# Kernel tuning notes

Hardware: AMD Instinct MI355X
Metric: run time of the kernel (lower is better)

## Reference

```python
import jax, jax.numpy as jnp
import numpy as np

B = 2
D = 256
NH = 8
DH = D // NH
LV = 4
NP_ = 4
NL = 6
DFF = 1024
SHAPES = [(112, 112), (56, 56), (28, 28), (14, 14)]
S = sum(h * w for h, w in SHAPES)


def setup_inputs() -> dict:
    key = jax.random.key(0)
    ks = iter(jax.random.split(key, 64))
    d = {}
    for i, (h, w) in enumerate(SHAPES):
        d[f"src{i}"] = jax.random.normal(next(ks), (B, D, h, w), jnp.float32)
        d[f"pos{i}"] = jax.random.normal(next(ks), (B, D, h, w), jnp.float32)

    def W(*shape, scale=0.02):
        return jax.random.normal(next(ks), shape, jnp.float32) * scale

    d["level_embed"] = W(LV, D, scale=1.0)
    d["off_w"] = W(NL, D, NH * LV * NP_ * 2)
    d["off_b"] = W(NL, NH * LV * NP_ * 2, scale=0.5)
    d["aw_w"] = W(NL, D, NH * LV * NP_)
    d["aw_b"] = jnp.zeros((NL, NH * LV * NP_), jnp.float32)
    d["val_w"] = W(NL, D, D)
    d["val_b"] = jnp.zeros((NL, D), jnp.float32)
    d["out_w"] = W(NL, D, D)
    d["out_b"] = jnp.zeros((NL, D), jnp.float32)
    d["ln1_s"] = jnp.ones((NL, D), jnp.float32)
    d["ln1_b"] = jnp.zeros((NL, D), jnp.float32)
    d["ff1_w"] = W(NL, D, DFF)
    d["ff1_b"] = jnp.zeros((NL, DFF), jnp.float32)
    d["ff2_w"] = W(NL, DFF, D)
    d["ff2_b"] = jnp.zeros((NL, D), jnp.float32)
    d["ln2_s"] = jnp.ones((NL, D), jnp.float32)
    d["ln2_b"] = jnp.zeros((NL, D), jnp.float32)
    return d


def _ln(x, s, b):
    m = jnp.mean(x, -1, keepdims=True)
    v = jnp.mean((x - m) ** 2, -1, keepdims=True)
    return (x - m) / jnp.sqrt(v + 1e-5) * s + b


def _bilinear(v, loc, Hl, Wl):
    # v: [N, DH, Hl, Wl]; loc: [N, Q, P, 2] in [0,1] (grid_sample align_corners=False, zero padding)
    N, Dh = v.shape[0], v.shape[1]
    Q, P = loc.shape[1], loc.shape[2]
    x = loc[..., 0] * Wl - 0.5
    y = loc[..., 1] * Hl - 0.5
    x0f = jnp.floor(x)
    y0f = jnp.floor(y)
    lx = x - x0f
    ly = y - y0f
    x0 = x0f.astype(jnp.int32)
    y0 = y0f.astype(jnp.int32)
    vf = v.reshape(N, Dh, Hl * Wl)

    def g(xi, yi):
        valid = (xi >= 0) & (xi < Wl) & (yi >= 0) & (yi < Hl)
        idx = (jnp.clip(yi, 0, Hl - 1) * Wl + jnp.clip(xi, 0, Wl - 1)).reshape(N, Q * P)
        out = jnp.take_along_axis(vf, idx[:, None, :], axis=2).reshape(N, Dh, Q, P)
        return out * valid[:, None].astype(v.dtype)

    w00 = ((1 - lx) * (1 - ly))[:, None]
    w10 = (lx * (1 - ly))[:, None]
    w01 = ((1 - lx) * ly)[:, None]
    w11 = (lx * ly)[:, None]
    return g(x0, y0) * w00 + g(x0 + 1, y0) * w10 + g(x0, y0 + 1) * w01 + g(x0 + 1, y0 + 1) * w11


def _ms_deform_attn(value, loc, attn):
    # value [B,S,NH,DH], loc [B,S,NH,LV,P,2], attn [B,S,NH,LV,P]
    out = jnp.zeros((B * NH, DH, S), value.dtype)
    s0 = 0
    for l, (Hl, Wl) in enumerate(SHAPES):
        vl = value[:, s0:s0 + Hl * Wl].reshape(B, Hl, Wl, NH, DH)
        vl = vl.transpose(0, 3, 4, 1, 2).reshape(B * NH, DH, Hl, Wl)
        ll = loc[:, :, :, l].transpose(0, 2, 1, 3, 4).reshape(B * NH, S, NP_, 2)
        al = attn[:, :, :, l].transpose(0, 2, 1, 3).reshape(B * NH, S, NP_)[:, None]
        out = out + (_bilinear(vl, ll, Hl, Wl) * al).sum(-1)
        s0 += Hl * Wl
    return out.reshape(B, NH * DH, S).transpose(0, 2, 1)


def _forward(srcs, poss, level_embed, off_w, off_b, aw_w, aw_b, val_w, val_b,
             out_w, out_b, ln1_s, ln1_b, ff1_w, ff1_b, ff2_w, ff2_b, ln2_s, ln2_b):
    src = jnp.concatenate([s.reshape(B, D, -1).transpose(0, 2, 1) for s in srcs], 1)
    pos = jnp.concatenate(
        [p.reshape(B, D, -1).transpose(0, 2, 1) + level_embed[i][None, None] for i, p in enumerate(poss)], 1)
    # reference points: padding masks are all-False => valid_ratios == 1
    refs = []
    for (Hl, Wl) in SHAPES:
        gy, gx = jnp.meshgrid((jnp.arange(Hl) + 0.5) / Hl, (jnp.arange(Wl) + 0.5) / Wl, indexing="ij")
        refs.append(jnp.stack([gx.ravel(), gy.ravel()], -1))
    ref = jnp.concatenate(refs, 0)  # [S, 2]
    normalizer = jnp.array([[w, h] for (h, w) in SHAPES], jnp.float32)  # [LV, 2] = (W, H)
    x = src
    for i in range(NL):
        q = x + pos
        off = (q @ off_w[i] + off_b[i]).reshape(B, S, NH, LV, NP_, 2)
        aw = jax.nn.softmax((q @ aw_w[i] + aw_b[i]).reshape(B, S, NH, LV * NP_), -1)
        aw = aw.reshape(B, S, NH, LV, NP_)
        val = (x @ val_w[i] + val_b[i]).reshape(B, S, NH, DH)
        loc = ref[None, :, None, None, None, :] + off / normalizer[None, None, None, :, None, :]
        attn_out = _ms_deform_attn(val, loc, aw) @ out_w[i] + out_b[i]
        x = _ln(x + attn_out, ln1_s[i], ln1_b[i])
        ff = jax.nn.relu(x @ ff1_w[i] + ff1_b[i]) @ ff2_w[i] + ff2_b[i]
        x = _ln(x + ff, ln2_s[i], ln2_b[i])
    return x


def reference(src0, src1, src2, src3, pos0, pos1, pos2, pos3, level_embed,
              off_w, off_b, aw_w, aw_b, val_w, val_b, out_w, out_b,
              ln1_s, ln1_b, ff1_w, ff1_b, ff2_w, ff2_b, ln2_s, ln2_b):
    memory = _forward([src0, src1, src2, src3], [pos0, pos1, pos2, pos3], level_embed,
                      off_w, off_b, aw_w, aw_b, val_w, val_b, out_w, out_b,
                      ln1_s, ln1_b, ff1_w, ff1_b, ff2_w, ff2_b, ln2_s, ln2_b)
    spatial_shapes = jnp.array(SHAPES, jnp.int32)
    level_start_index = jnp.concatenate(
        [jnp.zeros((1,), jnp.int32), jnp.cumsum(spatial_shapes.prod(1))[:-1].astype(jnp.int32)])
    return memory, spatial_shapes, level_start_index
```

## Files before the change

kernel.cpp:

```cpp
#include <hip/hip_runtime.h>


constexpr int kB  = 2;
constexpr int kD  = 256;
constexpr int kNH = 8;
constexpr int kLV = 4;
constexpr int kNP = 4;
constexpr int kNL = 6;
constexpr int kDFF = 1024;
constexpr int kS  = 16660;
constexpr int kM  = kB * kS;
constexpr int kMp = 33408;
constexpr int kMT = kMp / 128;
constexpr int kMT64 = kMp / 64;

typedef short bf16x8 __attribute__((ext_vector_type(8)));
typedef float f32x4  __attribute__((ext_vector_type(4)));

__device__ __forceinline__ unsigned short f2bf(float x) {
  union { float f; unsigned int u; } v; v.f = x;
  unsigned int r = v.u + 0x7FFFu + ((v.u >> 16) & 1u);
  return (unsigned short)(r >> 16);
}
__device__ __forceinline__ float bf2f(unsigned short u) {
  union { unsigned int u; float f; } v; v.u = ((unsigned int)u) << 16;
  return v.f;
}

#define GLOAD_LDS16(gp, lp)                                                    \
  __builtin_amdgcn_global_load_lds(                                            \
      (const __attribute__((address_space(1))) void*)(gp),                     \
      (__attribute__((address_space(3))) void*)(lp), 16, 0, 0)

__global__ __launch_bounds__(256) void build_xpos_k(
    const float* __restrict__ src, const float* __restrict__ pos,
    const float* __restrict__ lemb, float* __restrict__ xout,
    float* __restrict__ posout, unsigned short* __restrict__ xbf,
    unsigned short* __restrict__ qbf, int HW, int s0, int lvl)
{
  __shared__ float ts[32][33];
  __shared__ float tp[32][33];
  const int b  = blockIdx.z;
  const int p0 = blockIdx.x * 32, d0 = blockIdx.y * 32;
  const int tx = threadIdx.x, ty = threadIdx.y;
  for (int dd = ty; dd < 32; dd += 8) {
    int p = p0 + tx;
    if (p < HW) {
      size_t idx = ((size_t)b * kD + (d0 + dd)) * (size_t)HW + p;
      ts[dd][tx] = src[idx];
      tp[dd][tx] = pos[idx];
    }
  }
  __syncthreads();
  for (int pp = ty; pp < 32; pp += 8) {
    int p = p0 + pp, d = d0 + tx;
    if (p < HW) {
      size_t o = ((size_t)b * kS + (s0 + p)) * (size_t)kD + d;
      float x = ts[tx][pp];
      float pv = tp[tx][pp] + lemb[lvl * kD + d];
      xout[o] = x;
      posout[o] = pv;
      xbf[o] = f2bf(x);
      qbf[o] = f2bf(x + pv);
    }
  }
}

__global__ __launch_bounds__(256) void wconv_k(
    const float* __restrict__ W, unsigned short* __restrict__ Wt,
    int K, int N, int rowoff, int rowstotal)
{
  __shared__ float t[32][33];
  const int l = blockIdx.z;
  const int n0 = blockIdx.x * 32, k0 = blockIdx.y * 32;
  const int tx = threadIdx.x & 31, ty = threadIdx.x >> 5;
  const float* Wl = W + (size_t)l * K * N;
  unsigned short* Wtl = Wt + (size_t)l * rowstotal * K;
  for (int kk = ty; kk < 32; kk += 8)
    t[kk][tx] = Wl[(size_t)(k0 + kk) * N + n0 + tx];
  __syncthreads();
  for (int nn = ty; nn < 32; nn += 8)
    Wtl[(size_t)(rowoff + n0 + nn) * K + k0 + tx] = f2bf(t[tx][nn]);
}

__global__ __launch_bounds__(256) void biaspack_k(
    const float* __restrict__ ob, const float* __restrict__ ab,
    float* __restrict__ qb)
{
  int i = blockIdx.x * 256 + threadIdx.x;
  if (i >= kNL * 384) return;
  int l = i / 384, c = i - l * 384;
  qb[i] = (c < 256) ? ob[l * 256 + c] : ab[l * 128 + (c - 256)];
}

template<int RELU, int OUTBF>
__global__ __launch_bounds__(256) void hgemm_k(
    const unsigned short* __restrict__ A, const unsigned short* __restrict__ Bt,
    const float* __restrict__ bias, void* __restrict__ Cout, int N, int K)
{
  __shared__ unsigned short As[128 * 32];
  __shared__ unsigned short Bs[128 * 32];
  const int tid = threadIdx.x;
  const int bm = blockIdx.y * 128;
  const int bn = blockIdx.x * 128;
  const int lane = tid & 63;
  const int wave = tid >> 6;
  const int wr = (wave >> 1) * 64, wc = (wave & 1) * 64;
  const int l15 = lane & 15, l4 = lane >> 4;

  f32x4 acc[4][4] = {};

  const int c0 = tid, c1 = 256 + tid;
  const int r0 = c0 >> 2, kk0 = (c0 & 3) << 3;
  const int r1 = c1 >> 2, kk1 = (c1 & 3) << 3;
  const unsigned short* A0 = A + (size_t)(bm + r0) * K + kk0;
  const unsigned short* A1 = A + (size_t)(bm + r1) * K + kk1;
  const unsigned short* B0 = Bt + (size_t)(bn + r0) * K + kk0;
  const unsigned short* B1 = Bt + (size_t)(bn + r1) * K + kk1;

  for (int k0 = 0; k0 < K; k0 += 32) {
    GLOAD_LDS16(A0 + k0, (char*)As + c0 * 16);
    GLOAD_LDS16(A1 + k0, (char*)As + c1 * 16);
    GLOAD_LDS16(B0 + k0, (char*)Bs + c0 * 16);
    GLOAD_LDS16(B1 + k0, (char*)Bs + c1 * 16);
    __syncthreads();
    bf16x8 af[4], bfr[4];
#pragma unroll
    for (int m = 0; m < 4; ++m)
      af[m] = *(const bf16x8*)&As[(wr + m * 16 + l15) * 32 + l4 * 8];
#pragma unroll
    for (int n = 0; n < 4; ++n)
      bfr[n] = *(const bf16x8*)&Bs[(wc + n * 16 + l15) * 32 + l4 * 8];
#pragma unroll
    for (int m = 0; m < 4; ++m)
#pragma unroll
      for (int n = 0; n < 4; ++n)
        acc[m][n] = __builtin_amdgcn_mfma_f32_16x16x32_bf16(
            af[m], bfr[n], acc[m][n], 0, 0, 0);
    __syncthreads();
  }

#pragma unroll
  for (int n = 0; n < 4; ++n) {
    const int col = bn + wc + n * 16 + l15;
    const float bv = bias[col];
#pragma unroll
    for (int m = 0; m < 4; ++m) {
#pragma unroll
      for (int j = 0; j < 4; ++j) {
        const int row = bm + wr + m * 16 + l4 * 4 + j;
        float v = acc[m][n][j] + bv;
        if (RELU) v = fmaxf(v, 0.f);
        if (OUTBF)
          ((unsigned short*)Cout)[(size_t)row * N + col] = f2bf(v);
        else
          ((float*)Cout)[(size_t)row * N + col] = v;
      }
    }
  }
}

template<int OUTBF>
__global__ __launch_bounds__(256) void hgemm64_k(
    const unsigned short* __restrict__ A, const unsigned short* __restrict__ Bt,
    const float* __restrict__ bias, void* __restrict__ Cout, int N, int K)
{
  __shared__ unsigned short As[64 * 32];
  __shared__ unsigned short Bs[128 * 32];
  const int tid = threadIdx.x;
  const int bm = blockIdx.y * 64;
  const int bn = blockIdx.x * 128;
  const int lane = tid & 63;
  const int wave = tid >> 6;
  const int wr = (wave >> 1) * 32, wc = (wave & 1) * 64;
  const int l15 = lane & 15, l4 = lane >> 4;

  f32x4 acc[2][4] = {};

  const int ra = tid >> 2, ka = (tid & 3) << 3;
  const unsigned short* A0 = A + (size_t)(bm + ra) * K + ka;
  const int cb1 = 256 + tid;
  const unsigned short* B0 = Bt + (size_t)(bn + (tid >> 2)) * K + ((tid & 3) << 3);
  const unsigned short* B1 = Bt + (size_t)(bn + (cb1 >> 2)) * K + ((cb1 & 3) << 3);

  for (int k0 = 0; k0 < K; k0 += 32) {
    GLOAD_LDS16(A0 + k0, (char*)As + tid * 16);
    GLOAD_LDS16(B0 + k0, (char*)Bs + tid * 16);
    GLOAD_LDS16(B1 + k0, (char*)Bs + cb1 * 16);
    __syncthreads();
    bf16x8 af[2], bfr[4];
#pragma unroll
    for (int m = 0; m < 2; ++m)
      af[m] = *(const bf16x8*)&As[(wr + m * 16 + l15) * 32 + l4 * 8];
#pragma unroll
    for (int n = 0; n < 4; ++n)
      bfr[n] = *(const bf16x8*)&Bs[(wc + n * 16 + l15) * 32 + l4 * 8];
#pragma unroll
    for (int m = 0; m < 2; ++m)
#pragma unroll
      for (int n = 0; n < 4; ++n)
        acc[m][n] = __builtin_amdgcn_mfma_f32_16x16x32_bf16(
            af[m], bfr[n], acc[m][n], 0, 0, 0);
    __syncthreads();
  }

#pragma unroll
  for (int n = 0; n < 4; ++n) {
    const int col = bn + wc + n * 16 + l15;
    const float bv = bias[col];
#pragma unroll
    for (int m = 0; m < 2; ++m) {
#pragma unroll
      for (int j = 0; j < 4; ++j) {
        const int row = bm + wr + m * 16 + l4 * 4 + j;
        float v = acc[m][n][j] + bv;
        if (OUTBF)
          ((unsigned short*)Cout)[(size_t)row * N + col] = f2bf(v);
        else
          ((float*)Cout)[(size_t)row * N + col] = v;
      }
    }
  }
}

template<int WQ, int OUTDST>
__global__ __launch_bounds__(512) void hgemmln_k(
    const unsigned short* __restrict__ A, const unsigned short* __restrict__ Bt,
    const float* __restrict__ bias, const float* __restrict__ Rsd,
    const float* __restrict__ g, const float* __restrict__ beta,
    const float* __restrict__ posb, float* __restrict__ yout,
    unsigned short* __restrict__ xbf, unsigned short* __restrict__ qbf, int K)
{
  __shared__ unsigned short As[64 * 32];
  __shared__ unsigned short Bs[256 * 32];
  __shared__ float ssum[64][5];
  __shared__ float ssq[64][5];
  const int tid = threadIdx.x;
  const int bm = blockIdx.x * 64;
  const int lane = tid & 63;
  const int wave = tid >> 6;
  const int wr = (wave >> 2) * 32, wc = (wave & 3) * 64;
  const int l15 = lane & 15, l4 = lane >> 4;

  f32x4 acc[2][4] = {};

  const unsigned short* A0 = A + (size_t)(bm + (tid >> 2)) * K + ((tid & 3) << 3);
  const int cb1 = 512 + tid;
  const unsigned short* B0 = Bt + (size_t)(tid >> 2) * K + ((tid & 3) << 3);
  const unsigned short* B1 = Bt + (size_t)(cb1 >> 2) * K + ((cb1 & 3) << 3);

  for (int k0 = 0; k0 < K; k0 += 32) {
    if (tid < 256) GLOAD_LDS16(A0 + k0, (char*)As + tid * 16);
    GLOAD_LDS16(B0 + k0, (char*)Bs + tid * 16);
    GLOAD_LDS16(B1 + k0, (char*)Bs + cb1 * 16);
    __syncthreads();
    bf16x8 af[2], bfr[4];
#pragma unroll
    for (int m = 0; m < 2; ++m)
      af[m] = *(const bf16x8*)&As[(wr + m * 16 + l15) * 32 + l4 * 8];
#pragma unroll
    for (int n = 0; n < 4; ++n)
      bfr[n] = *(const bf16x8*)&Bs[(wc + n * 16 + l15) * 32 + l4 * 8];
#pragma unroll
    for (int m = 0; m < 2; ++m)
#pragma unroll
      for (int n = 0; n < 4; ++n)
        acc[m][n] = __builtin_amdgcn_mfma_f32_16x16x32_bf16(
            af[m], bfr[n], acc[m][n], 0, 0, 0);
    __syncthreads();
  }

  float bv[4], gv[4], btv[4];
#pragma unroll
  for (int n = 0; n < 4; ++n) {
    const int col = wc + n * 16 + l15;
    bv[n] = bias[col];
    gv[n] = g[col];
    btv[n] = beta[col];
  }
#pragma unroll
  for (int m = 0; m < 2; ++m) {
#pragma unroll
    for (int j = 0; j < 4; ++j) {
      const int row = bm + wr + m * 16 + l4 * 4 + j;
#pragma unroll
      for (int n = 0; n < 4; ++n)
        acc[m][n][j] += bv[n] + Rsd[(size_t)row * kD + wc + n * 16 + l15];
    }
  }
#pragma unroll
  for (int m = 0; m < 2; ++m) {
#pragma unroll
    for (int j = 0; j < 4; ++j) {
      float s = acc[m][0][j] + acc[m][1][j] + acc[m][2][j] + acc[m][3][j];
      float q = acc[m][0][j] * acc[m][0][j] + acc[m][1][j] * acc[m][1][j] +
                acc[m][2][j] * acc[m][2][j] + acc[m][3][j] * acc[m][3][j];
#pragma unroll
      for (int d2 = 1; d2 < 16; d2 <<= 1) {
        s += __shfl_xor(s, d2, 64);
        q += __shfl_xor(q, d2, 64);
      }
      if (l15 == 0) {
        const int r = wr + m * 16 + l4 * 4 + j;
        ssum[r][wave & 3] = s;
        ssq[r][wave & 3] = q;
      }
    }
  }
  __syncthreads();
#pragma unroll
  for (int m = 0; m < 2; ++m) {
#pragma unroll
    for (int j = 0; j < 4; ++j) {
      const int r = wr + m * 16 + l4 * 4 + j;
      const int row = bm + r;
      const float mean = (ssum[r][0] + ssum[r][1] + ssum[r][2] + ssum[r][3]) *
                         (1.0f / kD);
      const float var = (ssq[r][0] + ssq[r][1] + ssq[r][2] + ssq[r][3]) *
                        (1.0f / kD) - mean * mean;
      const float rstd = rsqrtf(var + 1e-5f);
      if (row < kM) {
#pragma unroll
        for (int n = 0; n < 4; ++n) {
          const int col = wc + n * 16 + l15;
          const float y = (acc[m][n][j] - mean) * rstd * gv[n] + btv[n];
          const size_t o = (size_t)row * kD + col;
          if (OUTDST) {
            yout[o] = y;
          } else {
            yout[o] = y;
            xbf[o] = f2bf(y);
            if (WQ) qbf[o] = f2bf(y + posb[o]);
          }
        }
      }
    }
  }
}

__global__ __launch_bounds__(256) void msdeform_k(
    const unsigned short* __restrict__ val, const float* __restrict__ qout,
    unsigned short* __restrict__ outbf)
{
  __shared__ int   sIdx[4][4][128];
  __shared__ float sW[4][4][128];
  const int bs0 = blockIdx.x * 4;
  const int tid = threadIdx.x;

#pragma unroll
  for (int it = 0; it < 2; ++it) {
    const int item = tid + it * 256;
    const int q = item >> 7;
    const int t = item & 127;
    const int bs = bs0 + q;
    const int b = bs / kS, s = bs - b * kS;
    const int l = (t & 15) >> 2;

    const float logit = qout[(size_t)bs * 384 + 256 + t];
    float mx = logit;
#pragma unroll
    for (int d2 = 1; d2 < 16; d2 <<= 1) mx = fmaxf(mx, __shfl_xor(mx, d2, 64));
    float e = __expf(logit - mx);
    float sm = e;
#pragma unroll
    for (int d2 = 1; d2 < 16; d2 <<= 1) sm += __shfl_xor(sm, d2, 64);
    const float a = e / sm;

    int ls, sideq;
    if (s < 12544)      { ls = s;         sideq = 112; }
    else if (s < 15680) { ls = s - 12544; sideq = 56;  }
    else if (s < 16464) { ls = s - 15680; sideq = 28;  }
    else                { ls = s - 16464; sideq = 14;  }
    const float rx = ((ls % sideq) + 0.5f) / (float)sideq;
    const float ry = ((ls / sideq) + 0.5f) / (float)sideq;

    const int side  = 112 >> l;
    const int start = (l >= 1 ? 12544 : 0) + (l >= 2 ? 3136 : 0) + (l >= 3 ? 784 : 0);
    const float ox = qout[(size_t)bs * 384 + t * 2 + 0];
    const float oy = qout[(size_t)bs * 384 + t * 2 + 1];
    const float xx = rx * side + ox - 0.5f;
    const float yy = ry * side + oy - 0.5f;
    const float xf = floorf(xx), yf = floorf(yy);
    const float lx = xx - xf, ly = yy - yf;
    const int x0 = (int)xf, y0 = (int)yf;
    const float w00 = (1.f - lx) * (1.f - ly) * a, w10 = lx * (1.f - ly) * a;
    const float w01 = (1.f - lx) * ly * a,         w11 = lx * ly * a;
    const bool xv0 = (unsigned)x0 < (unsigned)side, xv1 = (unsigned)(x0 + 1) < (unsigned)side;
    const bool yv0 = (unsigned)y0 < (unsigned)side, yv1 = (unsigned)(y0 + 1) < (unsigned)side;
    const int cx0 = min(max(x0, 0), side - 1), cx1 = min(max(x0 + 1, 0), side - 1);
    const int cy0 = min(max(y0, 0), side - 1), cy1 = min(max(y0 + 1, 0), side - 1);
    const int rowbase = b * kS + start;
    const int t2 = (t & 15) * 8 + (t >> 4);
    sIdx[0][q][t2] = rowbase + cy0 * side + cx0;
    sIdx[1][q][t2] = rowbase + cy0 * side + cx1;
    sIdx[2][q][t2] = rowbase + cy1 * side + cx0;
    sIdx[3][q][t2] = rowbase + cy1 * side + cx1;
    sW[0][q][t2] = (xv0 && yv0) ? w00 : 0.f;
    sW[1][q][t2] = (xv1 && yv0) ? w10 : 0.f;
    sW[2][q][t2] = (xv0 && yv1) ? w01 : 0.f;
    sW[3][q][t2] = (xv1 && yv1) ? w11 : 0.f;
  }
  __syncthreads();

  const int q  = tid >> 6;
  const int h  = (tid >> 3) & 7;
  const int l8 = tid & 7;
  const unsigned short* vb = val + h * 32 + l8 * 4;

  float a0 = 0.f, a1 = 0.f, a2 = 0.f, a3 = 0.f;
#pragma unroll
  for (int sp = 0; sp < 16; ++sp) {
    const int t2 = sp * 8 + h;
#pragma unroll
    for (int c = 0; c < 4; ++c) {
      const int r = sIdx[c][q][t2];
      const float w = sW[c][q][t2];
      const ushort4 v4 = *(const ushort4*)(vb + (size_t)r * 256);
      a0 = fmaf(w, bf2f(v4.x), a0);
      a1 = fmaf(w, bf2f(v4.y), a1);
      a2 = fmaf(w, bf2f(v4.z), a2);
      a3 = fmaf(w, bf2f(v4.w), a3);
    }
  }
  ushort4 o;
  o.x = f2bf(a0); o.y = f2bf(a1); o.z = f2bf(a2); o.w = f2bf(a3);
  *(ushort4*)(outbf + (size_t)(bs0 + q) * 256 + h * 32 + l8 * 4) = o;
}

__global__ void tail_k(float* __restrict__ out)
{
  if (threadIdx.x == 0) {
    const size_t n = (size_t)kM * kD;
    out[n + 0] = 112.f; out[n + 1] = 112.f;
    out[n + 2] = 56.f;  out[n + 3] = 56.f;
    out[n + 4] = 28.f;  out[n + 5] = 28.f;
    out[n + 6] = 14.f;  out[n + 7] = 14.f;
    out[n + 8] = 0.f;   out[n + 9] = 12544.f;
    out[n + 10] = 15680.f; out[n + 11] = 16464.f;
  }
}

extern "C" void kernel_launch(void* const* d_in, const int* in_sizes, int n_in,
                              void* d_out, int out_size, void* d_ws, size_t ws_size,
                              hipStream_t stream)
{
  const float* src[4] = {(const float*)d_in[0], (const float*)d_in[2],
                         (const float*)d_in[4], (const float*)d_in[6]};
  const float* pos[4] = {(const float*)d_in[1], (const float*)d_in[3],
                         (const float*)d_in[5], (const float*)d_in[7]};
  const float* lemb  = (const float*)d_in[8];
  const float* off_w = (const float*)d_in[9];
  const float* off_b = (const float*)d_in[10];
  const float* aw_w  = (const float*)d_in[11];
  const float* aw_b  = (const float*)d_in[12];
  const float* val_w = (const float*)d_in[13];
  const float* val_b = (const float*)d_in[14];
  const float* out_w = (const float*)d_in[15];
  const float* out_b = (const float*)d_in[16];
  const float* ln1_s = (const float*)d_in[17];
  const float* ln1_b = (const float*)d_in[18];
  const float* ff1_w = (const float*)d_in[19];
  const float* ff1_b = (const float*)d_in[20];
  const float* ff2_w = (const float*)d_in[21];
  const float* ff2_b = (const float*)d_in[22];
  const float* ln2_s = (const float*)d_in[23];
  const float* ln2_b = (const float*)d_in[24];

  const size_t SZ = (size_t)kMp * kD;
  float* ws   = (float*)d_ws;
  float* posb = (float*)d_out;
  float* xb   = ws;
  float* R    = ws + SZ;
  float* qout = R;
  unsigned short* valbf = (unsigned short*)(R + SZ + SZ / 2);
  unsigned short* attbf = (unsigned short*)(R + 2 * SZ);
  unsigned short* ffbf  = (unsigned short*)R;
  unsigned short* qbf   = (unsigned short*)(ws + 3 * SZ + SZ / 2);
  unsigned short* xbf   = qbf + SZ;
  unsigned short* wts   = (unsigned short*)(ws + 4 * SZ + SZ / 2);
  unsigned short* qwT  = wts;
  unsigned short* valT = qwT + kNL * 384 * 256;
  unsigned short* outT = valT + kNL * 256 * 256;
  unsigned short* ff1T = outT + kNL * 256 * 256;
  unsigned short* ff2T = ff1T + kNL * 1024 * 256;
  float* qbias = (float*)(ff2T + kNL * 256 * 1024);

  wconv_k<<<dim3(256 / 32, 256 / 32, kNL), 256, 0, stream>>>(off_w, qwT, 256, 256, 0, 384);
  wconv_k<<<dim3(128 / 32, 256 / 32, kNL), 256, 0, stream>>>(aw_w,  qwT, 256, 128, 256, 384);
  wconv_k<<<dim3(256 / 32, 256 / 32, kNL), 256, 0, stream>>>(val_w, valT, 256, 256, 0, 256);
  wconv_k<<<dim3(256 / 32, 256 / 32, kNL), 256, 0, stream>>>(out_w, outT, 256, 256, 0, 256);
  wconv_k<<<dim3(1024 / 32, 256 / 32, kNL), 256, 0, stream>>>(ff1_w, ff1T, 256, 1024, 0, 1024);
  wconv_k<<<dim3(256 / 32, 1024 / 32, kNL), 256, 0, stream>>>(ff2_w, ff2T, 1024, 256, 0, 256);
  biaspack_k<<<(kNL * 384 + 255) / 256, 256, 0, stream>>>(off_b, aw_b, qbias);

  const int sides[4]  = {112, 56, 28, 14};
  const int starts[4] = {0, 12544, 15680, 16464};
  for (int l = 0; l < 4; ++l) {
    int HW = sides[l] * sides[l];
    dim3 g((HW + 31) / 32, kD / 32, kB);
    build_xpos_k<<<g, dim3(32, 8), 0, stream>>>(src[l], pos[l], lemb, xb, posb,
                                                xbf, qbf, HW, starts[l], l);
  }

  const dim3 blk(256);
  for (int i = 0; i < kNL; ++i) {
    hgemm64_k<0><<<dim3(3, kMT64), blk, 0, stream>>>(
        qbf, qwT + (size_t)i * 384 * 256, qbias + i * 384, qout, 384, 256);
    hgemm64_k<1><<<dim3(2, kMT64), blk, 0, stream>>>(
        xbf, valT + (size_t)i * 256 * 256, val_b + i * 256, valbf, 256, 256);
    msdeform_k<<<kM / 4, blk, 0, stream>>>(valbf, qout, attbf);
    hgemmln_k<0, 0><<<kMT64, 512, 0, stream>>>(
        attbf, outT + (size_t)i * 256 * 256, out_b + i * 256, xb,
        ln1_s + i * kD, ln1_b + i * kD, nullptr, xb, xbf, nullptr, 256);
    hgemm_k<1, 1><<<dim3(8, kMT), blk, 0, stream>>>(
        xbf, ff1T + (size_t)i * 1024 * 256, ff1_b + i * 1024, ffbf, 1024, 256);
    if (i < kNL - 1) {
      hgemmln_k<1, 0><<<kMT64, 512, 0, stream>>>(
          ffbf, ff2T + (size_t)i * 256 * 1024, ff2_b + i * 256, xb,
          ln2_s + i * kD, ln2_b + i * kD, posb, xb, xbf, qbf, 1024);
    } else {
      hgemmln_k<0, 1><<<kMT64, 512, 0, stream>>>(
          ffbf, ff2T + (size_t)i * 256 * 1024, ff2_b + i * 256, xb,
          ln2_s + i * kD, ln2_b + i * kD, nullptr, (float*)d_out, nullptr,
          nullptr, 1024);
    }
  }

  tail_k<<<1, 64, 0, stream>>>((float*)d_out);
}
```

Before: 1.539 ms.

## Double-buffer LDS in hgemm64 and hgemmln, shrink LN-GEMM tile to 32 rows

Adds two-stage LDS double buffering to the 64-row GEMM and the GEMM+LayerNorm kernels, so the global-to-LDS load for the next K slice is issued before the current slice's MFMAs. This removes one barrier per iteration and hides load latency. The LN GEMM also changes from 64-row tiles with 512 threads to 32-row tiles with 256 threads, doubling the grid size but reloading the full 256-column B panel for every 32 rows. Both kernels use more LDS, and the LN GEMM fetches more B traffic in total.

```diff
diff --git a/kernel.cpp b/kernel.cpp
--- a/kernel.cpp
+++ b/kernel.cpp
@@ -13,6 +13,7 @@
 constexpr int kMp = 33408;
 constexpr int kMT = kMp / 128;
 constexpr int kMT64 = kMp / 64;
+constexpr int kMT32 = kMp / 32;
 
 typedef short bf16x8 __attribute__((ext_vector_type(8)));
 typedef float f32x4  __attribute__((ext_vector_type(4)));
@@ -165,8 +166,8 @@
     const unsigned short* __restrict__ A, const unsigned short* __restrict__ Bt,
     const float* __restrict__ bias, void* __restrict__ Cout, int N, int K)
 {
-  __shared__ unsigned short As[64 * 32];
-  __shared__ unsigned short Bs[128 * 32];
+  __shared__ unsigned short As[2][64 * 32];
+  __shared__ unsigned short Bs[2][128 * 32];
   const int tid = threadIdx.x;
   const int bm = blockIdx.y * 64;
   const int bn = blockIdx.x * 128;
@@ -177,24 +178,30 @@
 
   f32x4 acc[2][4] = {};
 
-  const int ra = tid >> 2, ka = (tid & 3) << 3;
-  const unsigned short* A0 = A + (size_t)(bm + ra) * K + ka;
+  const unsigned short* A0 = A + (size_t)(bm + (tid >> 2)) * K + ((tid & 3) << 3);
   const int cb1 = 256 + tid;
   const unsigned short* B0 = Bt + (size_t)(bn + (tid >> 2)) * K + ((tid & 3) << 3);
   const unsigned short* B1 = Bt + (size_t)(bn + (cb1 >> 2)) * K + ((cb1 & 3) << 3);
 
+#define STAGE64(buf, k0)                                                       \
+  do {                                                                         \
+    GLOAD_LDS16(A0 + (k0), (char*)As[buf] + tid * 16);                         \
+    GLOAD_LDS16(B0 + (k0), (char*)Bs[buf] + tid * 16);                         \
+    GLOAD_LDS16(B1 + (k0), (char*)Bs[buf] + cb1 * 16);                         \
+  } while (0)
+
+  STAGE64(0, 0);
+  __syncthreads();
+  int cur = 0;
   for (int k0 = 0; k0 < K; k0 += 32) {
-    GLOAD_LDS16(A0 + k0, (char*)As + tid * 16);
-    GLOAD_LDS16(B0 + k0, (char*)Bs + tid * 16);
-    GLOAD_LDS16(B1 + k0, (char*)Bs + cb1 * 16);
-    __syncthreads();
+    if (k0 + 32 < K) STAGE64(cur ^ 1, k0 + 32);
     bf16x8 af[2], bfr[4];
 #pragma unroll
     for (int m = 0; m < 2; ++m)
-      af[m] = *(const bf16x8*)&As[(wr + m * 16 + l15) * 32 + l4 * 8];
+      af[m] = *(const bf16x8*)&As[cur][(wr + m * 16 + l15) * 32 + l4 * 8];
 #pragma unroll
     for (int n = 0; n < 4; ++n)
-      bfr[n] = *(const bf16x8*)&Bs[(wc + n * 16 + l15) * 32 + l4 * 8];
+      bfr[n] = *(const bf16x8*)&Bs[cur][(wc + n * 16 + l15) * 32 + l4 * 8];
 #pragma unroll
     for (int m = 0; m < 2; ++m)
 #pragma unroll
@@ -202,7 +209,9 @@
         acc[m][n] = __builtin_amdgcn_mfma_f32_16x16x32_bf16(
             af[m], bfr[n], acc[m][n], 0, 0, 0);
     __syncthreads();
-  }
+    cur ^= 1;
+  }
+#undef STAGE64
 
 #pragma unroll
   for (int n = 0; n < 4; ++n) {
@@ -224,43 +233,53 @@
 }
 
 template<int WQ, int OUTDST>
-__global__ __launch_bounds__(512) void hgemmln_k(
+__global__ __launch_bounds__(256) void hgemmln_k(
     const unsigned short* __restrict__ A, const unsigned short* __restrict__ Bt,
     const float* __restrict__ bias, const float* __restrict__ Rsd,
     const float* __restrict__ g, const float* __restrict__ beta,
     const float* __restrict__ posb, float* __restrict__ yout,
     unsigned short* __restrict__ xbf, unsigned short* __restrict__ qbf, int K)
 {
-  __shared__ unsigned short As[64 * 32];
-  __shared__ unsigned short Bs[256 * 32];
-  __shared__ float ssum[64][5];
-  __shared__ float ssq[64][5];
+  __shared__ unsigned short As[2][32 * 32];
+  __shared__ unsigned short Bs[2][256 * 32];
+  __shared__ float ssum[32][5];
+  __shared__ float ssq[32][5];
   const int tid = threadIdx.x;
-  const int bm = blockIdx.x * 64;
+  const int bm = blockIdx.x * 32;
   const int lane = tid & 63;
   const int wave = tid >> 6;
-  const int wr = (wave >> 2) * 32, wc = (wave & 3) * 64;
+  const int wc = wave * 64;
   const int l15 = lane & 15, l4 = lane >> 4;
 
   f32x4 acc[2][4] = {};
 
-  const unsigned short* A0 = A + (size_t)(bm + (tid >> 2)) * K + ((tid & 3) << 3);
-  const int cb1 = 512 + tid;
-  const unsigned short* B0 = Bt + (size_t)(tid >> 2) * K + ((tid & 3) << 3);
-  const unsigned short* B1 = Bt + (size_t)(cb1 >> 2) * K + ((cb1 & 3) << 3);
-
+  const unsigned short* Aq = A + (size_t)(bm + (tid >> 2)) * K + ((tid & 3) << 3);
+  const unsigned short* Bq0 = Bt + (size_t)(0 * 64 + (tid >> 2)) * K + ((tid & 3) << 3);
+  const unsigned short* Bq1 = Bt + (size_t)(1 * 64 + (tid >> 2)) * K + ((tid & 3) << 3);
+  const unsigned short* Bq2 = Bt + (size_t)(2 * 64 + (tid >> 2)) * K + ((tid & 3) << 3);
+  const unsigned short* Bq3 = Bt + (size_t)(3 * 64 + (tid >> 2)) * K + ((tid & 3) << 3);
+
+#define STAGE_LN(buf, k0)                                                      \
+  do {                                                                         \
+    if (tid < 128) GLOAD_LDS16(Aq + (k0), (char*)As[buf] + tid * 16);          \
+    GLOAD_LDS16(Bq0 + (k0), (char*)Bs[buf] + (0 * 256 + tid) * 16);            \
+    GLOAD_LDS16(Bq1 + (k0), (char*)Bs[buf] + (1 * 256 + tid) * 16);            \
+    GLOAD_LDS16(Bq2 + (k0), (char*)Bs[buf] + (2 * 256 + tid) * 16);            \
+    GLOAD_LDS16(Bq3 + (k0), (char*)Bs[buf] + (3 * 256 + tid) * 16);            \
+  } while (0)
+
+  STAGE_LN(0, 0);
+  __syncthreads();
+  int cur = 0;
   for (int k0 = 0; k0 < K; k0 += 32) {
-    if (tid < 256) GLOAD_LDS16(A0 + k0, (char*)As + tid * 16);
-    GLOAD_LDS16(B0 + k0, (char*)Bs + tid * 16);
-    GLOAD_LDS16(B1 + k0, (char*)Bs + cb1 * 16);
-    __syncthreads();
+    if (k0 + 32 < K) STAGE_LN(cur ^ 1, k0 + 32);
     bf16x8 af[2], bfr[4];
 #pragma unroll
     for (int m = 0; m < 2; ++m)
-      af[m] = *(const bf16x8*)&As[(wr + m * 16 + l15) * 32 + l4 * 8];
+      af[m] = *(const bf16x8*)&As[cur][(m * 16 + l15) * 32 + l4 * 8];
 #pragma unroll
     for (int n = 0; n < 4; ++n)
-      bfr[n] = *(const bf16x8*)&Bs[(wc + n * 16 + l15) * 32 + l4 * 8];
+      bfr[n] = *(const bf16x8*)&Bs[cur][(wc + n * 16 + l15) * 32 + l4 * 8];
 #pragma unroll
     for (int m = 0; m < 2; ++m)
 #pragma unroll
@@ -268,7 +287,9 @@
         acc[m][n] = __builtin_amdgcn_mfma_f32_16x16x32_bf16(
             af[m], bfr[n], acc[m][n], 0, 0, 0);
     __syncthreads();
-  }
+    cur ^= 1;
+  }
+#undef STAGE_LN
 
   float bv[4], gv[4], btv[4];
 #pragma unroll
@@ -282,7 +303,7 @@
   for (int m = 0; m < 2; ++m) {
 #pragma unroll
     for (int j = 0; j < 4; ++j) {
-      const int row = bm + wr + m * 16 + l4 * 4 + j;
+      const int row = bm + m * 16 + l4 * 4 + j;
 #pragma unroll
       for (int n = 0; n < 4; ++n)
         acc[m][n][j] += bv[n] + Rsd[(size_t)row * kD + wc + n * 16 + l15];
@@ -301,9 +322,9 @@
         q += __shfl_xor(q, d2, 64);
       }
       if (l15 == 0) {
-        const int r = wr + m * 16 + l4 * 4 + j;
-        ssum[r][wave & 3] = s;
-        ssq[r][wave & 3] = q;
+        const int r = m * 16 + l4 * 4 + j;
+        ssum[r][wave] = s;
+        ssq[r][wave] = q;
       }
     }
   }
@@ -312,7 +333,7 @@
   for (int m = 0; m < 2; ++m) {
 #pragma unroll
     for (int j = 0; j < 4; ++j) {
-      const int r = wr + m * 16 + l4 * 4 + j;
+      const int r = m * 16 + l4 * 4 + j;
       const int row = bm + r;
       const float mean = (ssum[r][0] + ssum[r][1] + ssum[r][2] + ssum[r][3]) *
                          (1.0f / kD);
@@ -509,17 +530,17 @@
     hgemm64_k<1><<<dim3(2, kMT64), blk, 0, stream>>>(
         xbf, valT + (size_t)i * 256 * 256, val_b + i * 256, valbf, 256, 256);
     msdeform_k<<<kM / 4, blk, 0, stream>>>(valbf, qout, attbf);
-    hgemmln_k<0, 0><<<kMT64, 512, 0, stream>>>(
+    hgemmln_k<0, 0><<<kMT32, blk, 0, stream>>>(
         attbf, outT + (size_t)i * 256 * 256, out_b + i * 256, xb,
         ln1_s + i * kD, ln1_b + i * kD, nullptr, xb, xbf, nullptr, 256);
     hgemm_k<1, 1><<<dim3(8, kMT), blk, 0, stream>>>(
         xbf, ff1T + (size_t)i * 1024 * 256, ff1_b + i * 1024, ffbf, 1024, 256);
     if (i < kNL - 1) {
-      hgemmln_k<1, 0><<<kMT64, 512, 0, stream>>>(
+      hgemmln_k<1, 0><<<kMT32, blk, 0, stream>>>(
           ffbf, ff2T + (size_t)i * 256 * 1024, ff2_b + i * 256, xb,
           ln2_s + i * kD, ln2_b + i * kD, posb, xb, xbf, qbf, 1024);
     } else {
-      hgemmln_k<0, 1><<<kMT64, 512, 0, stream>>>(
+      hgemmln_k<0, 1><<<kMT32, blk, 0, stream>>>(
           ffbf, ff2T + (size_t)i * 256 * 1024, ff2_b + i * 256, xb,
           ln2_s + i * kD, ln2_b + i * kD, nullptr, (float*)d_out, nullptr,
           nullptr, 1024);
```

Measured after the change: 1.510 ms. About the same (-1.9%).
